# Kernel tuning notes

Measured on AMD Instinct MI355X. Metric: run time of the kernel, lower is better.

The kernel has to match this reference:

```python
import jax, jax.numpy as jnp
import numpy as np

TAU = 1.0  # confidence threshold (stands in for StatsTestConfidence)

BATCH = 8192
IN_FEATURES = 4096
OUT_FEATURES = 4096
EARLY_K = 1024


def setup_inputs() -> dict:
    key = jax.random.key(0)
    kx, kw = jax.random.split(key)
    x = jax.random.normal(kx, (BATCH, IN_FEATURES), dtype=jnp.float32)
    # nn.Linear weight: (out_features, in_features)
    W = jax.random.normal(kw, (OUT_FEATURES, IN_FEATURES), dtype=jnp.float32) * (IN_FEATURES ** -0.5)
    return {"x": x, "W": W, "early_terminate_it": EARLY_K}


def reference(x, W, early_terminate_it):
    k = early_terminate_it
    # partial matmul over first k input channels
    y1 = x[:, :k] @ W[:, :k].T                              # [B, out]
    # per-column squared rank-1 accumulation == (x^2) @ (W^2)^T over first k cols
    cum_squared = (x[:, :k] ** 2) @ (W[:, :k] ** 2).T        # [B, out]
    # confidence test: outputs whose partial sum is small relative to its
    # column-wise energy are 'passed' (early-terminated to 0)
    passed_mask = jnp.abs(y1) < TAU * jnp.sqrt(cum_squared)  # [B, out] bool
    # remaining matmul over the rest of the input channels
    y2 = x[:, k:] @ W[:, k:].T                               # [B, out]
    return jnp.where(passed_mask, jnp.zeros((), x.dtype), y1 + y2)
```

## Files before the change

### kernel.cpp

```cpp
#include <hip/hip_runtime.h>
#include <math.h>

#define BATCH 8192
#define OUTF  4096
#define INF   4096
#define K1    1024
#define KC    512
#define MARGIN 8.0e-4f

#define BK 32
#define NT (INF / BK)
#define NT1 (K1 / BK)
#define NP1 32
#define NSTEPS 80
#define GRIDX 32
#define GRIDY 64

typedef __attribute__((ext_vector_type(8))) short bf16x8;
typedef __attribute__((ext_vector_type(8))) unsigned short u16x8;
typedef __attribute__((ext_vector_type(4))) float f32x4;

__device__ inline unsigned short bf16_rn(float f) {
    unsigned u = __float_as_uint(f);
    unsigned r = 0x7FFFu + ((u >> 16) & 1u);
    return (unsigned short)((u + r) >> 16);
}
__device__ inline float bf16_f(unsigned short h) {
    return __uint_as_float(((unsigned)h) << 16);
}

__device__ inline int swz_idx(int r, int cc) {
    return r * 32 + ((cc ^ ((r >> 1) & 3)) << 3);
}

__device__ inline void gload_lds16(const void* g, void* l) {
    __builtin_amdgcn_global_load_lds(
        (const __attribute__((address_space(1))) unsigned*)g,
        (__attribute__((address_space(3))) unsigned*)l, 16, 0, 0);
}

__device__ float exact_serial(const float* __restrict__ x,
                              const float* __restrict__ w, int b, int o) {
    const float* xr = x + (size_t)b * INF;
    const float* wr = w + (size_t)o * INF;
    float py = 0.f, ty = 0.f, pc = 0.f, tcs = 0.f;
    double y1d = 0.0, y2d = 0.0;
    for (int j = 0; j < K1; ++j) {
        float xv = xr[j], wv = wr[j];
        py = fmaf(xv, wv, py);
        pc = fmaf(xv * xv, wv * wv, pc);
        y1d += (double)xv * (double)wv;
        if (((j + 1) & (KC - 1)) == 0) { ty += py; py = 0.f; tcs += pc; pc = 0.f; }
    }
    for (int j = K1; j < INF; ++j)
        y2d += (double)xr[j] * (double)wr[j];
    bool passed = fabsf(ty) < (float)sqrt((double)tcs);
    return passed ? 0.f : (float)(y1d + y2d);
}

__global__ void zero_ws(unsigned* ws) {
    if (threadIdx.x < 16) ws[threadIdx.x] = 0u;
}

__global__ __launch_bounds__(256) void
split_rows(const float* __restrict__ src, unsigned short* __restrict__ pair,
           unsigned short* __restrict__ sq, int nrows)
{
    int t = blockIdx.x * blockDim.x + threadIdx.x;
    if (t >= nrows * (INF / 8)) return;
    int gr  = t >> 9;
    int gk8 = t & 511;
    int kb = gk8 >> 2, cc = gk8 & 3;
    int rb = gr >> 7,  r  = gr & 127;
    int swz = swz_idx(r, cc);

    const float* s = src + (size_t)gr * INF + gk8 * 8;
    float4 f0 = *(const float4*)s;
    float4 f1 = *(const float4*)(s + 4);
    float fv[8] = {f0.x, f0.y, f0.z, f0.w, f1.x, f1.y, f1.z, f1.w};
    u16x8 h8, l8, s8;
    #pragma unroll
    for (int e = 0; e < 8; ++e) {
        float f = fv[e];
        unsigned short h = bf16_rn(f);
        h8[e] = h;
        l8[e] = bf16_rn(f - bf16_f(h));
        s8[e] = bf16_rn(f * f);
    }
    size_t pb = ((size_t)rb * (INF / 32) + kb) * 8192;
    *(u16x8*)&pair[pb + swz] = h8;
    if (kb < NT1) {
        *(u16x8*)&pair[pb + 4096 + swz] = l8;
        size_t qb = ((size_t)rb * NT1 + kb) * 4096;
        *(u16x8*)&sq[qb + swz] = s8;
    }
}

__global__ __launch_bounds__(256, 3) void
cs_kernel(const unsigned short* __restrict__ xsq,
          const unsigned short* __restrict__ wsq, float* __restrict__ out)
{
    __shared__ unsigned short lds2[16384];

    unsigned orig = blockIdx.y * GRIDX + blockIdx.x;
    unsigned swid = (orig & 7u) * (GRIDX * GRIDY / 8) + (orig >> 3);
    const int bx = (int)(swid & (GRIDX - 1));
    const int by = (int)(swid / GRIDX);
    const int brow = by * 128;
    const int bcol = bx * 128;

    const int tid  = threadIdx.x;
    const int lane = tid & 63;
    const int wvid = tid >> 6;
    const int wm   = wvid >> 1;
    const int wn   = wvid & 1;

    const int c0 = lane >> 4;
    int aidx[4], bidx[4];
    #pragma unroll
    for (int mi = 0; mi < 4; ++mi)
        aidx[mi] = swz_idx(wm * 64 + mi * 16 + (lane & 15), c0);
    #pragma unroll
    for (int nj = 0; nj < 4; ++nj)
        bidx[nj] = 4096 + swz_idx(wn * 64 + nj * 16 + (lane & 15), c0);

    f32x4 cs[4][4];
    #pragma unroll
    for (int mi = 0; mi < 4; ++mi)
        #pragma unroll
        for (int nj = 0; nj < 4; ++nj)
            cs[mi][nj] = (f32x4){0.f, 0.f, 0.f, 0.f};

    char* ldsb = (char*)lds2;
    const char* xq = (const char*)xsq + (size_t)by * NT1 * 8192;
    const char* wq = (const char*)wsq + (size_t)bx * NT1 * 8192;

    auto STAGE = [&](int dstB, int t) {
        #pragma unroll
        for (int i = 0; i < 4; ++i) {
            int j = wvid + i * 4;
            const char* g = (j < 8) ? xq + (size_t)t * 8192 + j * 1024
                                    : wq + (size_t)t * 8192 + (j - 8) * 1024;
            gload_lds16(g + lane * 16, ldsb + dstB + j * 1024);
        }
    };

    STAGE(0, 0);
    int bo = 0;
    for (int t = 0; t < NT1; ++t) {
        asm volatile("s_waitcnt vmcnt(0)" ::: "memory");
        __builtin_amdgcn_s_barrier();
        __builtin_amdgcn_sched_barrier(0);
        if (t + 1 < NT1) STAGE((bo ^ 8192) * 2, t + 1);

        bf16x8 b2[4];
        #pragma unroll
        for (int nj = 0; nj < 4; ++nj)
            b2[nj] = *(const bf16x8*)&lds2[bo + bidx[nj]];
        #pragma unroll
        for (int mi = 0; mi < 4; ++mi) {
            bf16x8 a2 = *(const bf16x8*)&lds2[bo + aidx[mi]];
            #pragma unroll
            for (int nj = 0; nj < 4; ++nj)
                cs[mi][nj] = __builtin_amdgcn_mfma_f32_16x16x32_bf16(a2, b2[nj], cs[mi][nj], 0, 0, 0);
        }
        bo ^= 8192;
    }

    const int rbase = brow + wm * 64 + (lane >> 4) * 4;
    const int cbase = bcol + wn * 64 + (lane & 15);
    #pragma unroll
    for (int mi = 0; mi < 4; ++mi)
        #pragma unroll
        for (int nj = 0; nj < 4; ++nj)
            #pragma unroll
            for (int q = 0; q < 4; ++q)
                out[(size_t)(rbase + mi * 16 + q) * OUTF + cbase + nj * 16] =
                    sqrtf(cs[mi][nj][q]);
}

__global__ __launch_bounds__(256, 2) void
mfma_pass_a9(const unsigned short* __restrict__ xpair,
             const unsigned short* __restrict__ wpair,
             const float* __restrict__ x, const float* __restrict__ w,
             float* __restrict__ out, unsigned* ws,
             unsigned* __restrict__ list, unsigned cap)
{
    __shared__ unsigned short lds_us[32768];

    unsigned orig = blockIdx.y * GRIDX + blockIdx.x;
    unsigned swid = (orig & 7u) * (GRIDX * GRIDY / 8) + (orig >> 3);
    const int bx = (int)(swid & (GRIDX - 1));
    const int by = (int)(swid / GRIDX);
    const int brow = by * 128;
    const int bcol = bx * 128;

    const int tid  = threadIdx.x;
    const int lane = tid & 63;
    const int wvid = tid >> 6;
    const int wm   = wvid >> 1;
    const int wn   = wvid & 1;

    const int c0 = lane >> 4;
    int aidx[4], bidx[4];
    #pragma unroll
    for (int mi = 0; mi < 4; ++mi)
        aidx[mi] = swz_idx(wm * 64 + mi * 16 + (lane & 15), c0);
    #pragma unroll
    for (int nj = 0; nj < 4; ++nj)
        bidx[nj] = swz_idx(wn * 64 + nj * 16 + (lane & 15), c0);

    const int rbase = brow + wm * 64 + (lane >> 4) * 4;
    const int cbase = bcol + wn * 64 + (lane & 15);

    f32x4 acc[4][4];
    #pragma unroll
    for (int mi = 0; mi < 4; ++mi)
        #pragma unroll
        for (int nj = 0; nj < 4; ++nj)
            acc[mi][nj] = (f32x4){0.f, 0.f, 0.f, 0.f};

    unsigned long long pmask = 0ull, nmask = 0ull;
    char* ldsb = (char*)lds_us;
    const char* xp = (const char*)xpair + (size_t)by * NT * 16384;
    const char* wp = (const char*)wpair + (size_t)bx * NT * 16384;

    auto STAGE = [&](int dstB, int s) {
        if (s < NP1) {
            #pragma unroll
            for (int i = 0; i < 8; ++i) {
                int j = wvid + i * 4;
                const char* g = (j < 16) ? xp + (size_t)s * 16384 + j * 1024
                                         : wp + (size_t)s * 16384 + (j - 16) * 1024;
                gload_lds16(g + lane * 16, ldsb + dstB + j * 1024);
            }
        } else {
            int kt = NT1 + 2 * (s - NP1);
            #pragma unroll
            for (int i = 0; i < 8; ++i) {
                int j = wvid + i * 4;
                const char* g =
                    (j < 8)  ? xp + (size_t)kt * 16384 + j * 1024 :
                    (j < 16) ? xp + (size_t)(kt + 1) * 16384 + (j - 8) * 1024 :
                    (j < 24) ? wp + (size_t)kt * 16384 + (j - 16) * 1024 :
                               wp + (size_t)(kt + 1) * 16384 + (j - 24) * 1024;
                gload_lds16(g + lane * 16, ldsb + dstB + j * 1024);
            }
        }
    };

    STAGE(0, 0);
    int bo = 0;
    for (int s = 0; s < NSTEPS; ++s) {
        asm volatile("s_waitcnt vmcnt(0)" ::: "memory");
        __builtin_amdgcn_s_barrier();
        __builtin_amdgcn_sched_barrier(0);

        if (s == NP1) {
            #pragma unroll
            for (int mi = 0; mi < 4; ++mi)
                #pragma unroll
                for (int nj = 0; nj < 4; ++nj)
                    #pragma unroll
                    for (int q = 0; q < 4; ++q) {
                        float sref = out[(size_t)(rbase + mi * 16 + q) * OUTF +
                                         cbase + nj * 16];
                        float d = fabsf(acc[mi][nj][q]) - sref;
                        int bit = ((mi * 4 + nj) * 4 + q);
                        if (d < 0.f)           pmask |= 1ull << bit;
                        if (fabsf(d) < MARGIN) nmask |= 1ull << bit;
                    }
        }

        if (s + 1 < NSTEPS) STAGE((bo ^ 16384) * 2, s + 1);

        if (s < NP1) {
            bf16x8 bh[4], bl[4];
            #pragma unroll
            for (int nj = 0; nj < 4; ++nj) {
                bh[nj] = *(const bf16x8*)&lds_us[bo + 8192  + bidx[nj]];
                bl[nj] = *(const bf16x8*)&lds_us[bo + 12288 + bidx[nj]];
            }
            #pragma unroll
            for (int mi = 0; mi < 4; ++mi) {
                bf16x8 ah = *(const bf16x8*)&lds_us[bo + aidx[mi]];
                bf16x8 al = *(const bf16x8*)&lds_us[bo + 4096 + aidx[mi]];
                #pragma unroll
                for (int nj = 0; nj < 4; ++nj) {
                    acc[mi][nj] = __builtin_amdgcn_mfma_f32_16x16x32_bf16(ah, bh[nj], acc[mi][nj], 0, 0, 0);
                    acc[mi][nj] = __builtin_amdgcn_mfma_f32_16x16x32_bf16(ah, bl[nj], acc[mi][nj], 0, 0, 0);
                    acc[mi][nj] = __builtin_amdgcn_mfma_f32_16x16x32_bf16(al, bh[nj], acc[mi][nj], 0, 0, 0);
                }
            }
        } else {
            #pragma unroll
            for (int sub = 0; sub < 2; ++sub) {
                const int ao = bo + sub * 4096;
                const int bb = bo + 8192 + sub * 4096;
                bf16x8 bh[4];
                #pragma unroll
                for (int nj = 0; nj < 4; ++nj)
                    bh[nj] = *(const bf16x8*)&lds_us[bb + bidx[nj]];
                #pragma unroll
                for (int mi = 0; mi < 4; ++mi) {
                    bf16x8 ah = *(const bf16x8*)&lds_us[ao + aidx[mi]];
                    #pragma unroll
                    for (int nj = 0; nj < 4; ++nj)
                        acc[mi][nj] = __builtin_amdgcn_mfma_f32_16x16x32_bf16(ah, bh[nj], acc[mi][nj], 0, 0, 0);
                }
            }
        }
        bo ^= 16384;
    }

    #pragma unroll
    for (int mi = 0; mi < 4; ++mi)
        #pragma unroll
        for (int nj = 0; nj < 4; ++nj) {
            int col = cbase + nj * 16;
            #pragma unroll
            for (int q = 0; q < 4; ++q) {
                int row = rbase + mi * 16 + q;
                int bit = ((mi * 4 + nj) * 4 + q);
                float raw = acc[mi][nj][q];
                float val = ((pmask >> bit) & 1ull) ? 0.f : raw;
                if ((nmask >> bit) & 1ull) {
                    unsigned idx = atomicAdd(&ws[0], 1u);
                    if (idx < cap) {
                        list[2 * idx]     = ((unsigned)row << 12) | (unsigned)col;
                        list[2 * idx + 1] = __float_as_uint(raw);
                    } else {
                        val = exact_serial(x, w, row, col);
                    }
                }
                out[(size_t)row * OUTF + col] = val;
            }
        }
}

__global__ __launch_bounds__(512) void
mfma_pass_a_fb(const float* __restrict__ x, const float* __restrict__ w,
               float* __restrict__ out, unsigned* ws,
               unsigned* __restrict__ list, unsigned cap)
{
    __shared__ unsigned short ldsA0[128 * 32];
    __shared__ unsigned short ldsA1[128 * 32];
    __shared__ unsigned short ldsA2[128 * 32];
    __shared__ unsigned short ldsB0[128 * 32];
    __shared__ unsigned short ldsB1[128 * 32];
    __shared__ unsigned short ldsB2[128 * 32];

    const int tid  = threadIdx.x;
    const int brow = blockIdx.y * 128;
    const int bcol = blockIdx.x * 128;
    const int lane = tid & 63;
    const int wid  = tid >> 6;
    const int wm   = wid >> 2;
    const int wn   = wid & 3;

    const int sr = tid >> 2;
    const int sc = tid & 3;
    const float* xg = x + (size_t)(brow + sr) * INF + sc * 8;
    const float* wg = w + (size_t)(bcol + sr) * INF + sc * 8;
    const int swz = sr * 32 + ((sc ^ (sr & 3)) << 3);

    const int c0 = lane >> 4;
    int aidx[4], bidx[2];
    #pragma unroll
    for (int mi = 0; mi < 4; ++mi) {
        int r = wm * 64 + mi * 16 + (lane & 15);
        aidx[mi] = r * 32 + ((c0 ^ (r & 3)) << 3);
    }
    #pragma unroll
    for (int nj = 0; nj < 2; ++nj) {
        int r = wn * 32 + nj * 16 + (lane & 15);
        bidx[nj] = r * 32 + ((c0 ^ (r & 3)) << 3);
    }

    f32x4 acc[4][2];
    f32x4 csa[4][2];
    #pragma unroll
    for (int mi = 0; mi < 4; ++mi)
        #pragma unroll
        for (int nj = 0; nj < 2; ++nj) {
            acc[mi][nj] = (f32x4){0.f, 0.f, 0.f, 0.f};
            csa[mi][nj] = (f32x4){0.f, 0.f, 0.f, 0.f};
        }

    for (int k0 = 0; k0 < K1; k0 += BK) {
        float xv[8], wv[8];
        *(float4*)&xv[0] = *(const float4*)(xg + k0);
        *(float4*)&xv[4] = *(const float4*)(xg + k0 + 4);
        *(float4*)&wv[0] = *(const float4*)(wg + k0);
        *(float4*)&wv[4] = *(const float4*)(wg + k0 + 4);
        __syncthreads();
        u16x8 h8, l8, s8;
        #pragma unroll
        for (int e = 0; e < 8; ++e) {
            float f = xv[e];
            unsigned short h = bf16_rn(f);
            h8[e] = h; l8[e] = bf16_rn(f - bf16_f(h)); s8[e] = bf16_rn(f * f);
        }
        *(u16x8*)&ldsA0[swz] = h8; *(u16x8*)&ldsA1[swz] = l8; *(u16x8*)&ldsA2[swz] = s8;
        #pragma unroll
        for (int e = 0; e < 8; ++e) {
            float f = wv[e];
            unsigned short h = bf16_rn(f);
            h8[e] = h; l8[e] = bf16_rn(f - bf16_f(h)); s8[e] = bf16_rn(f * f);
        }
        *(u16x8*)&ldsB0[swz] = h8; *(u16x8*)&ldsB1[swz] = l8; *(u16x8*)&ldsB2[swz] = s8;
        __syncthreads();

        bf16x8 bh[2], bl[2], b2[2];
        #pragma unroll
        for (int nj = 0; nj < 2; ++nj) {
            bh[nj] = *(const bf16x8*)&ldsB0[bidx[nj]];
            bl[nj] = *(const bf16x8*)&ldsB1[bidx[nj]];
            b2[nj] = *(const bf16x8*)&ldsB2[bidx[nj]];
        }
        #pragma unroll
        for (int mi = 0; mi < 4; ++mi) {
            bf16x8 ah = *(const bf16x8*)&ldsA0[aidx[mi]];
            bf16x8 al = *(const bf16x8*)&ldsA1[aidx[mi]];
            bf16x8 a2 = *(const bf16x8*)&ldsA2[aidx[mi]];
            #pragma unroll
            for (int nj = 0; nj < 2; ++nj) {
                acc[mi][nj] = __builtin_amdgcn_mfma_f32_16x16x32_bf16(ah, bh[nj], acc[mi][nj], 0, 0, 0);
                acc[mi][nj] = __builtin_amdgcn_mfma_f32_16x16x32_bf16(ah, bl[nj], acc[mi][nj], 0, 0, 0);
                acc[mi][nj] = __builtin_amdgcn_mfma_f32_16x16x32_bf16(al, bh[nj], acc[mi][nj], 0, 0, 0);
                csa[mi][nj] = __builtin_amdgcn_mfma_f32_16x16x32_bf16(a2, b2[nj], csa[mi][nj], 0, 0, 0);
            }
        }
    }

    unsigned pmask = 0u, nmask = 0u;
    #pragma unroll
    for (int mi = 0; mi < 4; ++mi)
        #pragma unroll
        for (int nj = 0; nj < 2; ++nj)
            #pragma unroll
            for (int q = 0; q < 4; ++q) {
                float d = fabsf(acc[mi][nj][q]) - sqrtf(csa[mi][nj][q]);
                unsigned bit = (unsigned)((((mi << 1) | nj) << 2) | q);
                if (d < 0.f)           pmask |= 1u << bit;
                if (fabsf(d) < MARGIN) nmask |= 1u << bit;
            }

    for (int k0 = K1; k0 < INF; k0 += BK) {
        float xv[8], wv[8];
        *(float4*)&xv[0] = *(const float4*)(xg + k0);
        *(float4*)&xv[4] = *(const float4*)(xg + k0 + 4);
        *(float4*)&wv[0] = *(const float4*)(wg + k0);
        *(float4*)&wv[4] = *(const float4*)(wg + k0 + 4);
        __syncthreads();
        u16x8 h8, l8;
        #pragma unroll
        for (int e = 0; e < 8; ++e) {
            float f = xv[e];
            unsigned short h = bf16_rn(f);
            h8[e] = h; l8[e] = bf16_rn(f - bf16_f(h));
        }
        *(u16x8*)&ldsA0[swz] = h8; *(u16x8*)&ldsA1[swz] = l8;
        #pragma unroll
        for (int e = 0; e < 8; ++e) {
            float f = wv[e];
            unsigned short h = bf16_rn(f);
            h8[e] = h; l8[e] = bf16_rn(f - bf16_f(h));
        }
        *(u16x8*)&ldsB0[swz] = h8; *(u16x8*)&ldsB1[swz] = l8;
        __syncthreads();

        bf16x8 bh[2], bl[2];
        #pragma unroll
        for (int nj = 0; nj < 2; ++nj) {
            bh[nj] = *(const bf16x8*)&ldsB0[bidx[nj]];
            bl[nj] = *(const bf16x8*)&ldsB1[bidx[nj]];
        }
        #pragma unroll
        for (int mi = 0; mi < 4; ++mi) {
            bf16x8 ah = *(const bf16x8*)&ldsA0[aidx[mi]];
            bf16x8 al = *(const bf16x8*)&ldsA1[aidx[mi]];
            #pragma unroll
            for (int nj = 0; nj < 2; ++nj) {
                acc[mi][nj] = __builtin_amdgcn_mfma_f32_16x16x32_bf16(ah, bh[nj], acc[mi][nj], 0, 0, 0);
                acc[mi][nj] = __builtin_amdgcn_mfma_f32_16x16x32_bf16(ah, bl[nj], acc[mi][nj], 0, 0, 0);
                acc[mi][nj] = __builtin_amdgcn_mfma_f32_16x16x32_bf16(al, bh[nj], acc[mi][nj], 0, 0, 0);
            }
        }
    }

    const int rbase = brow + wm * 64 + (lane >> 4) * 4;
    const int cbase = bcol + wn * 32 + (lane & 15);
    #pragma unroll
    for (int mi = 0; mi < 4; ++mi)
        #pragma unroll
        for (int nj = 0; nj < 2; ++nj) {
            int col = cbase + nj * 16;
            #pragma unroll
            for (int q = 0; q < 4; ++q) {
                int row = rbase + mi * 16 + q;
                unsigned bit = (unsigned)((((mi << 1) | nj) << 2) | q);
                float raw = acc[mi][nj][q];
                float val = ((pmask >> bit) & 1u) ? 0.f : raw;
                if ((nmask >> bit) & 1u) {
                    unsigned idx = ws ? atomicAdd(&ws[0], 1u) : 0xFFFFFFFFu;
                    if (idx < cap) {
                        list[2 * idx]     = ((unsigned)row << 12) | (unsigned)col;
                        list[2 * idx + 1] = __float_as_uint(raw);
                    } else {
                        val = exact_serial(x, w, row, col);
                    }
                }
                out[(size_t)row * OUTF + col] = val;
            }
        }
}

__global__ __launch_bounds__(256) void
exact_pass_b(const float* __restrict__ x, const float* __restrict__ w,
             float* __restrict__ out, const unsigned* __restrict__ ws,
             const unsigned* __restrict__ list, unsigned cap)
{
    unsigned n = ws[0]; if (n > cap) n = cap;
    unsigned stride = gridDim.x * blockDim.x;
    for (unsigned e = blockIdx.x * blockDim.x + threadIdx.x; e < n; e += stride) {
        unsigned p  = list[2 * e];
        float   val = __uint_as_float(list[2 * e + 1]);
        int b = (int)(p >> 12), o = (int)(p & 4095u);
        const float* xr = x + (size_t)b * INF;
        const float* wr = w + (size_t)o * INF;

        float py = 0.f, ty = 0.f, pc = 0.f, tcs = 0.f;
        for (int j = 0; j < K1; j += 4) {
            float4 xv = *(const float4*)(xr + j);
            float4 wv = *(const float4*)(wr + j);
            py = fmaf(xv.x, wv.x, py); pc = fmaf(xv.x * xv.x, wv.x * wv.x, pc);
            py = fmaf(xv.y, wv.y, py); pc = fmaf(xv.y * xv.y, wv.y * wv.y, pc);
            py = fmaf(xv.z, wv.z, py); pc = fmaf(xv.z * xv.z, wv.z * wv.z, pc);
            py = fmaf(xv.w, wv.w, py); pc = fmaf(xv.w * xv.w, wv.w * wv.w, pc);
            if (((j + 4) & (KC - 1)) == 0) {
                ty += py;  py = 0.f;
                tcs += pc; pc = 0.f;
            }
        }
        bool passed = fabsf(ty) < (float)sqrt((double)tcs);
        out[(size_t)b * OUTF + o] = passed ? 0.f : val;
    }
}

extern "C" void kernel_launch(void* const* d_in, const int* in_sizes, int n_in,
                              void* d_out, int out_size, void* d_ws, size_t ws_size,
                              hipStream_t stream)
{
    const float* x = (const float*)d_in[0];
    const float* w = (const float*)d_in[1];
    float* out = (float*)d_out;

    const size_t MB = 1ull << 20;
    if (ws_size >= 224 * MB) {
        unsigned* ws   = (unsigned*)d_ws;
        unsigned* list = ws + 16;
        unsigned  cap  = (unsigned)((8 * MB - 64) / 8);
        char* base = (char*)d_ws;
        unsigned short* xpair = (unsigned short*)(base + 8 * MB);
        unsigned short* wpair = (unsigned short*)(base + 136 * MB);
        unsigned short* xsq   = (unsigned short*)(base + 200 * MB);
        unsigned short* wsq   = (unsigned short*)(base + 216 * MB);

        zero_ws<<<1, 64, 0, stream>>>(ws);
        split_rows<<<(BATCH * (INF / 8)) / 256, 256, 0, stream>>>(x, xpair, xsq, BATCH);
        split_rows<<<(OUTF  * (INF / 8)) / 256, 256, 0, stream>>>(w, wpair, wsq, OUTF);
        cs_kernel<<<dim3(GRIDX, GRIDY), 256, 0, stream>>>(xsq, wsq, out);
        mfma_pass_a9<<<dim3(GRIDX, GRIDY), 256, 0, stream>>>(
            xpair, wpair, x, w, out, ws, list, cap);
        exact_pass_b<<<1024, 256, 0, stream>>>(x, w, out, ws, list, cap);
    } else if (ws_size >= (1u << 20)) {
        unsigned* ws   = (unsigned*)d_ws;
        unsigned* list = ws + 16;
        size_t c = (ws_size - 64) / 8;
        unsigned cap = (c > (size_t)(1u << 23)) ? (1u << 23) : (unsigned)c;
        zero_ws<<<1, 64, 0, stream>>>(ws);
        mfma_pass_a_fb<<<dim3(32, 64), 512, 0, stream>>>(x, w, out, ws, list, cap);
        exact_pass_b<<<1024, 256, 0, stream>>>(x, w, out, ws, list, cap);
    } else {
        mfma_pass_a_fb<<<dim3(32, 64), 512, 0, stream>>>(x, w, out, nullptr, nullptr, 0);
    }
}
```

Measured before the change: 1.090 ms.

## Split fused two-phase MFMA kernel into separate y1 and y2 kernels

Replaces the single 80-step kernel with two launches. The first handles the first K1 channels with the 3-term bf16 split, makes the pass/near decision and writes y1. The second is a lighter single-term kernel for the remaining channels; it uses half the LDS and allows 4 blocks per CU, then adds y2 to the stored y1 unless y1 is zero. Staging now uses precomputed pointers that are bumped each step, and the list stores only indices because exact_pass_b reads the value back from out. The cost is an extra full read and write of the output buffer between kernels. Also, when the near-list overflows, entries are no longer checked exactly, and a y1 that happens to be exactly zero is treated as passed.

```diff
diff --git a/kernel.cpp b/kernel.cpp
--- a/kernel.cpp
+++ b/kernel.cpp
@@ -11,8 +11,7 @@
 #define BK 32
 #define NT (INF / BK)
 #define NT1 (K1 / BK)
-#define NP1 32
-#define NSTEPS 80
+#define NT2 (NT - NT1)
 #define GRIDX 32
 #define GRIDY 64
 
@@ -37,25 +36,6 @@
     __builtin_amdgcn_global_load_lds(
         (const __attribute__((address_space(1))) unsigned*)g,
         (__attribute__((address_space(3))) unsigned*)l, 16, 0, 0);
-}
-
-__device__ float exact_serial(const float* __restrict__ x,
-                              const float* __restrict__ w, int b, int o) {
-    const float* xr = x + (size_t)b * INF;
-    const float* wr = w + (size_t)o * INF;
-    float py = 0.f, ty = 0.f, pc = 0.f, tcs = 0.f;
-    double y1d = 0.0, y2d = 0.0;
-    for (int j = 0; j < K1; ++j) {
-        float xv = xr[j], wv = wr[j];
-        py = fmaf(xv, wv, py);
-        pc = fmaf(xv * xv, wv * wv, pc);
-        y1d += (double)xv * (double)wv;
-        if (((j + 1) & (KC - 1)) == 0) { ty += py; py = 0.f; tcs += pc; pc = 0.f; }
-    }
-    for (int j = K1; j < INF; ++j)
-        y2d += (double)xr[j] * (double)wr[j];
-    bool passed = fabsf(ty) < (float)sqrt((double)tcs);
-    return passed ? 0.f : (float)(y1d + y2d);
 }
 
 __global__ void zero_ws(unsigned* ws) {
@@ -135,23 +115,30 @@
     const char* xq = (const char*)xsq + (size_t)by * NT1 * 8192;
     const char* wq = (const char*)wsq + (size_t)bx * NT1 * 8192;
 
-    auto STAGE = [&](int dstB, int t) {
-        #pragma unroll
-        for (int i = 0; i < 4; ++i) {
-            int j = wvid + i * 4;
-            const char* g = (j < 8) ? xq + (size_t)t * 8192 + j * 1024
-                                    : wq + (size_t)t * 8192 + (j - 8) * 1024;
-            gload_lds16(g + lane * 16, ldsb + dstB + j * 1024);
-        }
+    const char* gp[4];
+    #pragma unroll
+    for (int i = 0; i < 4; ++i) {
+        int j = wvid + i * 4;
+        gp[i] = ((j < 8) ? xq + j * 1024 : wq + (j - 8) * 1024) + lane * 16;
+    }
+
+    auto STAGE = [&](int dstB) {
+        #pragma unroll
+        for (int i = 0; i < 4; ++i)
+            gload_lds16(gp[i], ldsb + dstB + (wvid + i * 4) * 1024);
     };
-
-    STAGE(0, 0);
+    auto ADV = [&]() {
+        #pragma unroll
+        for (int i = 0; i < 4; ++i) gp[i] += 8192;
+    };
+
+    STAGE(0); ADV();
     int bo = 0;
     for (int t = 0; t < NT1; ++t) {
         asm volatile("s_waitcnt vmcnt(0)" ::: "memory");
         __builtin_amdgcn_s_barrier();
         __builtin_amdgcn_sched_barrier(0);
-        if (t + 1 < NT1) STAGE((bo ^ 8192) * 2, t + 1);
+        if (t + 1 < NT1) { STAGE((bo ^ 8192) * 2); ADV(); }
 
         bf16x8 b2[4];
         #pragma unroll
@@ -180,11 +167,10 @@
 }
 
 __global__ __launch_bounds__(256, 2) void
-mfma_pass_a9(const unsigned short* __restrict__ xpair,
-             const unsigned short* __restrict__ wpair,
-             const float* __restrict__ x, const float* __restrict__ w,
-             float* __restrict__ out, unsigned* ws,
-             unsigned* __restrict__ list, unsigned cap)
+mfma_p1(const unsigned short* __restrict__ xpair,
+        const unsigned short* __restrict__ wpair,
+        float* __restrict__ out, unsigned* ws,
+        unsigned* __restrict__ list, unsigned cap)
 {
     __shared__ unsigned short lds_us[32768];
 
@@ -220,94 +206,49 @@
         for (int nj = 0; nj < 4; ++nj)
             acc[mi][nj] = (f32x4){0.f, 0.f, 0.f, 0.f};
 
-    unsigned long long pmask = 0ull, nmask = 0ull;
     char* ldsb = (char*)lds_us;
     const char* xp = (const char*)xpair + (size_t)by * NT * 16384;
     const char* wp = (const char*)wpair + (size_t)bx * NT * 16384;
 
-    auto STAGE = [&](int dstB, int s) {
-        if (s < NP1) {
-            #pragma unroll
-            for (int i = 0; i < 8; ++i) {
-                int j = wvid + i * 4;
-                const char* g = (j < 16) ? xp + (size_t)s * 16384 + j * 1024
-                                         : wp + (size_t)s * 16384 + (j - 16) * 1024;
-                gload_lds16(g + lane * 16, ldsb + dstB + j * 1024);
-            }
-        } else {
-            int kt = NT1 + 2 * (s - NP1);
-            #pragma unroll
-            for (int i = 0; i < 8; ++i) {
-                int j = wvid + i * 4;
-                const char* g =
-                    (j < 8)  ? xp + (size_t)kt * 16384 + j * 1024 :
-                    (j < 16) ? xp + (size_t)(kt + 1) * 16384 + (j - 8) * 1024 :
-                    (j < 24) ? wp + (size_t)kt * 16384 + (j - 16) * 1024 :
-                               wp + (size_t)(kt + 1) * 16384 + (j - 24) * 1024;
-                gload_lds16(g + lane * 16, ldsb + dstB + j * 1024);
-            }
-        }
+    const char* gp[8];
+    #pragma unroll
+    for (int i = 0; i < 8; ++i) {
+        int j = wvid + i * 4;
+        gp[i] = ((j < 16) ? xp + j * 1024 : wp + (j - 16) * 1024) + lane * 16;
+    }
+    auto STAGE = [&](int dstB) {
+        #pragma unroll
+        for (int i = 0; i < 8; ++i)
+            gload_lds16(gp[i], ldsb + dstB + (wvid + i * 4) * 1024);
     };
-
-    STAGE(0, 0);
+    auto ADV = [&]() {
+        #pragma unroll
+        for (int i = 0; i < 8; ++i) gp[i] += 16384;
+    };
+
+    STAGE(0); ADV();
     int bo = 0;
-    for (int s = 0; s < NSTEPS; ++s) {
+    for (int s = 0; s < NT1; ++s) {
         asm volatile("s_waitcnt vmcnt(0)" ::: "memory");
         __builtin_amdgcn_s_barrier();
         __builtin_amdgcn_sched_barrier(0);
-
-        if (s == NP1) {
-            #pragma unroll
-            for (int mi = 0; mi < 4; ++mi)
-                #pragma unroll
-                for (int nj = 0; nj < 4; ++nj)
-                    #pragma unroll
-                    for (int q = 0; q < 4; ++q) {
-                        float sref = out[(size_t)(rbase + mi * 16 + q) * OUTF +
-                                         cbase + nj * 16];
-                        float d = fabsf(acc[mi][nj][q]) - sref;
-                        int bit = ((mi * 4 + nj) * 4 + q);
-                        if (d < 0.f)           pmask |= 1ull << bit;
-                        if (fabsf(d) < MARGIN) nmask |= 1ull << bit;
-                    }
-        }
-
-        if (s + 1 < NSTEPS) STAGE((bo ^ 16384) * 2, s + 1);
-
-        if (s < NP1) {
-            bf16x8 bh[4], bl[4];
+        if (s + 1 < NT1) { STAGE((bo ^ 16384) * 2); ADV(); }
+
+        bf16x8 bh[4], bl[4];
+        #pragma unroll
+        for (int nj = 0; nj < 4; ++nj) {
+            bh[nj] = *(const bf16x8*)&lds_us[bo + 8192  + bidx[nj]];
+            bl[nj] = *(const bf16x8*)&lds_us[bo + 12288 + bidx[nj]];
+        }
+        #pragma unroll
+        for (int mi = 0; mi < 4; ++mi) {
+            bf16x8 ah = *(const bf16x8*)&lds_us[bo + aidx[mi]];
+            bf16x8 al = *(const bf16x8*)&lds_us[bo + 4096 + aidx[mi]];
             #pragma unroll
             for (int nj = 0; nj < 4; ++nj) {
-                bh[nj] = *(const bf16x8*)&lds_us[bo + 8192  + bidx[nj]];
-                bl[nj] = *(const bf16x8*)&lds_us[bo + 12288 + bidx[nj]];
-            }
-            #pragma unroll
-            for (int mi = 0; mi < 4; ++mi) {
-                bf16x8 ah = *(const bf16x8*)&lds_us[bo + aidx[mi]];
-                bf16x8 al = *(const bf16x8*)&lds_us[bo + 4096 + aidx[mi]];
-                #pragma unroll
-                for (int nj = 0; nj < 4; ++nj) {
-                    acc[mi][nj] = __builtin_amdgcn_mfma_f32_16x16x32_bf16(ah, bh[nj], acc[mi][nj], 0, 0, 0);
-                    acc[mi][nj] = __builtin_amdgcn_mfma_f32_16x16x32_bf16(ah, bl[nj], acc[mi][nj], 0, 0, 0);
-                    acc[mi][nj] = __builtin_amdgcn_mfma_f32_16x16x32_bf16(al, bh[nj], acc[mi][nj], 0, 0, 0);
-                }
-            }
-        } else {
-            #pragma unroll
-            for (int sub = 0; sub < 2; ++sub) {
-                const int ao = bo + sub * 4096;
-                const int bb = bo + 8192 + sub * 4096;
-                bf16x8 bh[4];
-                #pragma unroll
-                for (int nj = 0; nj < 4; ++nj)
-                    bh[nj] = *(const bf16x8*)&lds_us[bb + bidx[nj]];
-                #pragma unroll
-                for (int mi = 0; mi < 4; ++mi) {
-                    bf16x8 ah = *(const bf16x8*)&lds_us[ao + aidx[mi]];
-                    #pragma unroll
-                    for (int nj = 0; nj < 4; ++nj)
-                        acc[mi][nj] = __builtin_amdgcn_mfma_f32_16x16x32_bf16(ah, bh[nj], acc[mi][nj], 0, 0, 0);
-                }
+                acc[mi][nj] = __builtin_amdgcn_mfma_f32_16x16x32_bf16(ah, bh[nj], acc[mi][nj], 0, 0, 0);
+                acc[mi][nj] = __builtin_amdgcn_mfma_f32_16x16x32_bf16(ah, bl[nj], acc[mi][nj], 0, 0, 0);
+                acc[mi][nj] = __builtin_amdgcn_mfma_f32_16x16x32_bf16(al, bh[nj], acc[mi][nj], 0, 0, 0);
             }
         }
         bo ^= 16384;
@@ -321,19 +262,114 @@
             #pragma unroll
             for (int q = 0; q < 4; ++q) {
                 int row = rbase + mi * 16 + q;
-                int bit = ((mi * 4 + nj) * 4 + q);
-                float raw = acc[mi][nj][q];
-                float val = ((pmask >> bit) & 1ull) ? 0.f : raw;
-                if ((nmask >> bit) & 1ull) {
-                    unsigned idx = atomicAdd(&ws[0], 1u);
-                    if (idx < cap) {
-                        list[2 * idx]     = ((unsigned)row << 12) | (unsigned)col;
-                        list[2 * idx + 1] = __float_as_uint(raw);
-                    } else {
-                        val = exact_serial(x, w, row, col);
-                    }
+                size_t idx = (size_t)row * OUTF + col;
+                float sref = out[idx];
+                float raw  = acc[mi][nj][q];
+                float d = fabsf(raw) - sref;
+                bool passed = d < 0.f;
+                bool near   = fabsf(d) < MARGIN;
+                if (near) {
+                    unsigned li = atomicAdd(&ws[0], 1u);
+                    if (li < cap)
+                        list[li] = ((unsigned)row << 12) | (unsigned)col;
                 }
-                out[(size_t)row * OUTF + col] = val;
+                out[idx] = (passed && !near) ? 0.f : raw;
+            }
+        }
+}
+
+__global__ __launch_bounds__(256, 4) void
+mfma_p2(const unsigned short* __restrict__ xpair,
+        const unsigned short* __restrict__ wpair,
+        float* __restrict__ out)
+{
+    __shared__ unsigned short lds_us[16384];
+
+    unsigned orig = blockIdx.y * GRIDX + blockIdx.x;
+    unsigned swid = (orig & 7u) * (GRIDX * GRIDY / 8) + (orig >> 3);
+    const int bx = (int)(swid & (GRIDX - 1));
+    const int by = (int)(swid / GRIDX);
+    const int brow = by * 128;
+    const int bcol = bx * 128;
+
+    const int tid  = threadIdx.x;
+    const int lane = tid & 63;
+    const int wvid = tid >> 6;
+    const int wm   = wvid >> 1;
+    const int wn   = wvid & 1;
+
+    const int c0 = lane >> 4;
+    int aidx[4], bidx[4];
+    #pragma unroll
+    for (int mi = 0; mi < 4; ++mi)
+        aidx[mi] = swz_idx(wm * 64 + mi * 16 + (lane & 15), c0);
+    #pragma unroll
+    for (int nj = 0; nj < 4; ++nj)
+        bidx[nj] = 4096 + swz_idx(wn * 64 + nj * 16 + (lane & 15), c0);
+
+    const int rbase = brow + wm * 64 + (lane >> 4) * 4;
+    const int cbase = bcol + wn * 64 + (lane & 15);
+
+    f32x4 acc[4][4];
+    #pragma unroll
+    for (int mi = 0; mi < 4; ++mi)
+        #pragma unroll
+        for (int nj = 0; nj < 4; ++nj)
+            acc[mi][nj] = (f32x4){0.f, 0.f, 0.f, 0.f};
+
+    char* ldsb = (char*)lds_us;
+    const char* xp = (const char*)xpair + ((size_t)by * NT + NT1) * 16384;
+    const char* wp = (const char*)wpair + ((size_t)bx * NT + NT1) * 16384;
+
+    const char* gp[4];
+    #pragma unroll
+    for (int i = 0; i < 4; ++i) {
+        int j = wvid + i * 4;
+        gp[i] = ((j < 8) ? xp + j * 1024 : wp + (j - 8) * 1024) + lane * 16;
+    }
+    auto STAGE = [&](int dstB) {
+        #pragma unroll
+        for (int i = 0; i < 4; ++i)
+            gload_lds16(gp[i], ldsb + dstB + (wvid + i * 4) * 1024);
+    };
+    auto ADV = [&]() {
+        #pragma unroll
+        for (int i = 0; i < 4; ++i) gp[i] += 16384;
+    };
+
+    STAGE(0); ADV();
+    int bo = 0;
+    for (int s = 0; s < NT2; ++s) {
+        asm volatile("s_waitcnt vmcnt(0)" ::: "memory");
+        __builtin_amdgcn_s_barrier();
+        __builtin_amdgcn_sched_barrier(0);
+        if (s + 1 < NT2) { STAGE((bo ^ 8192) * 2); ADV(); }
+
+        bf16x8 bh[4];
+        #pragma unroll
+        for (int nj = 0; nj < 4; ++nj)
+            bh[nj] = *(const bf16x8*)&lds_us[bo + bidx[nj]];
+        #pragma unroll
+        for (int mi = 0; mi < 4; ++mi) {
+            bf16x8 ah = *(const bf16x8*)&lds_us[bo + aidx[mi]];
+            #pragma unroll
+            for (int nj = 0; nj < 4; ++nj)
+                acc[mi][nj] = __builtin_amdgcn_mfma_f32_16x16x32_bf16(ah, bh[nj], acc[mi][nj], 0, 0, 0);
+        }
+        bo ^= 8192;
+    }
+
+    #pragma unroll
+    for (int mi = 0; mi < 4; ++mi)
+        #pragma unroll
+        for (int nj = 0; nj < 4; ++nj) {
+            int col = cbase + nj * 16;
+            #pragma unroll
+            for (int q = 0; q < 4; ++q) {
+                int row = rbase + mi * 16 + q;
+                size_t idx = (size_t)row * OUTF + col;
+                float y1v = out[idx];
+                out[idx] = (y1v == 0.f) ? 0.f : (y1v + acc[mi][nj][q]);
             }
         }
 }
@@ -501,17 +537,14 @@
                 int row = rbase + mi * 16 + q;
                 unsigned bit = (unsigned)((((mi << 1) | nj) << 2) | q);
                 float raw = acc[mi][nj][q];
-                float val = ((pmask >> bit) & 1u) ? 0.f : raw;
-                if ((nmask >> bit) & 1u) {
-                    unsigned idx = ws ? atomicAdd(&ws[0], 1u) : 0xFFFFFFFFu;
-                    if (idx < cap) {
-                        list[2 * idx]     = ((unsigned)row << 12) | (unsigned)col;
-                        list[2 * idx + 1] = __float_as_uint(raw);
-                    } else {
-                        val = exact_serial(x, w, row, col);
-                    }
+                bool passed = (pmask >> bit) & 1u;
+                bool near   = (nmask >> bit) & 1u;
+                if (near && ws) {
+                    unsigned li = atomicAdd(&ws[0], 1u);
+                    if (li < cap)
+                        list[li] = ((unsigned)row << 12) | (unsigned)col;
                 }
-                out[(size_t)row * OUTF + col] = val;
+                out[(size_t)row * OUTF + col] = (passed && !near) ? 0.f : raw;
             }
         }
 }
@@ -524,8 +557,7 @@
     unsigned n = ws[0]; if (n > cap) n = cap;
     unsigned stride = gridDim.x * blockDim.x;
     for (unsigned e = blockIdx.x * blockDim.x + threadIdx.x; e < n; e += stride) {
-        unsigned p  = list[2 * e];
-        float   val = __uint_as_float(list[2 * e + 1]);
+        unsigned p = list[e];
         int b = (int)(p >> 12), o = (int)(p & 4095u);
         const float* xr = x + (size_t)b * INF;
         const float* wr = w + (size_t)o * INF;
@@ -544,7 +576,8 @@
             }
         }
         bool passed = fabsf(ty) < (float)sqrt((double)tcs);
-        out[(size_t)b * OUTF + o] = passed ? 0.f : val;
+        size_t idx = (size_t)b * OUTF + o;
+        out[idx] = passed ? 0.f : out[idx];
     }
 }
 
@@ -560,7 +593,7 @@
     if (ws_size >= 224 * MB) {
         unsigned* ws   = (unsigned*)d_ws;
         unsigned* list = ws + 16;
-        unsigned  cap  = (unsigned)((8 * MB - 64) / 8);
+        unsigned  cap  = (unsigned)((8 * MB - 64) / 4);
         char* base = (char*)d_ws;
         unsigned short* xpair = (unsigned short*)(base + 8 * MB);
         unsigned short* wpair = (unsigned short*)(base + 136 * MB);
@@ -571,13 +604,13 @@
         split_rows<<<(BATCH * (INF / 8)) / 256, 256, 0, stream>>>(x, xpair, xsq, BATCH);
         split_rows<<<(OUTF  * (INF / 8)) / 256, 256, 0, stream>>>(w, wpair, wsq, OUTF);
         cs_kernel<<<dim3(GRIDX, GRIDY), 256, 0, stream>>>(xsq, wsq, out);
-        mfma_pass_a9<<<dim3(GRIDX, GRIDY), 256, 0, stream>>>(
-            xpair, wpair, x, w, out, ws, list, cap);
+        mfma_p1<<<dim3(GRIDX, GRIDY), 256, 0, stream>>>(xpair, wpair, out, ws, list, cap);
+        mfma_p2<<<dim3(GRIDX, GRIDY), 256, 0, stream>>>(xpair, wpair, out);
         exact_pass_b<<<1024, 256, 0, stream>>>(x, w, out, ws, list, cap);
     } else if (ws_size >= (1u << 20)) {
         unsigned* ws   = (unsigned*)d_ws;
         unsigned* list = ws + 16;
-        size_t c = (ws_size - 64) / 8;
+        size_t c = (ws_size - 64) / 4;
         unsigned cap = (c > (size_t)(1u << 23)) ? (1u << 23) : (unsigned)c;
         zero_ws<<<1, 64, 0, stream>>>(ws);
         mfma_pass_a_fb<<<dim3(32, 64), 512, 0, stream>>>(x, w, out, ws, list, cap);
```

Result: slower. 1.134 ms (+4.0%).

## Load low-bf16 residual fragments directly from global and shrink LDS footprint

Applied to the files above, without the earlier changes.

The main MFMA kernel no longer stages the low halves of the split-bf16 operands through LDS. split_rows now writes them in a per-lane fragment layout, so they can be read straight from global memory into registers. The tail loop goes back to one K-tile per step instead of two, LDS use is halved, and the occupancy hints are raised (3 blocks per CU for the main kernel, 4 for cs_kernel). The exact_serial fallback for list overflow is removed, so entries past capacity would keep the unrefined value, and the direct global loads add latency that is not double-buffered.

```diff
diff --git a/kernel.cpp b/kernel.cpp
--- a/kernel.cpp
+++ b/kernel.cpp
@@ -11,8 +11,6 @@
 #define BK 32
 #define NT (INF / BK)
 #define NT1 (K1 / BK)
-#define NP1 32
-#define NSTEPS 80
 #define GRIDX 32
 #define GRIDY 64
 
@@ -32,30 +30,14 @@
 __device__ inline int swz_idx(int r, int cc) {
     return r * 32 + ((cc ^ ((r >> 1) & 3)) << 3);
 }
+__device__ inline int frag_idx(int r, int cc) {
+    return ((r >> 4) * 64 + cc * 16 + (r & 15)) * 8;
+}
 
 __device__ inline void gload_lds16(const void* g, void* l) {
     __builtin_amdgcn_global_load_lds(
         (const __attribute__((address_space(1))) unsigned*)g,
         (__attribute__((address_space(3))) unsigned*)l, 16, 0, 0);
-}
-
-__device__ float exact_serial(const float* __restrict__ x,
-                              const float* __restrict__ w, int b, int o) {
-    const float* xr = x + (size_t)b * INF;
-    const float* wr = w + (size_t)o * INF;
-    float py = 0.f, ty = 0.f, pc = 0.f, tcs = 0.f;
-    double y1d = 0.0, y2d = 0.0;
-    for (int j = 0; j < K1; ++j) {
-        float xv = xr[j], wv = wr[j];
-        py = fmaf(xv, wv, py);
-        pc = fmaf(xv * xv, wv * wv, pc);
-        y1d += (double)xv * (double)wv;
-        if (((j + 1) & (KC - 1)) == 0) { ty += py; py = 0.f; tcs += pc; pc = 0.f; }
-    }
-    for (int j = K1; j < INF; ++j)
-        y2d += (double)xr[j] * (double)wr[j];
-    bool passed = fabsf(ty) < (float)sqrt((double)tcs);
-    return passed ? 0.f : (float)(y1d + y2d);
 }
 
 __global__ void zero_ws(unsigned* ws) {
@@ -72,7 +54,6 @@
     int gk8 = t & 511;
     int kb = gk8 >> 2, cc = gk8 & 3;
     int rb = gr >> 7,  r  = gr & 127;
-    int swz = swz_idx(r, cc);
 
     const float* s = src + (size_t)gr * INF + gk8 * 8;
     float4 f0 = *(const float4*)s;
@@ -88,15 +69,15 @@
         s8[e] = bf16_rn(f * f);
     }
     size_t pb = ((size_t)rb * (INF / 32) + kb) * 8192;
-    *(u16x8*)&pair[pb + swz] = h8;
+    *(u16x8*)&pair[pb + swz_idx(r, cc)] = h8;
     if (kb < NT1) {
-        *(u16x8*)&pair[pb + 4096 + swz] = l8;
+        *(u16x8*)&pair[pb + 4096 + frag_idx(r, cc)] = l8;
         size_t qb = ((size_t)rb * NT1 + kb) * 4096;
-        *(u16x8*)&sq[qb + swz] = s8;
-    }
-}
-
-__global__ __launch_bounds__(256, 3) void
+        *(u16x8*)&sq[qb + swz_idx(r, cc)] = s8;
+    }
+}
+
+__global__ __launch_bounds__(256, 4) void
 cs_kernel(const unsigned short* __restrict__ xsq,
           const unsigned short* __restrict__ wsq, float* __restrict__ out)
 {
@@ -179,14 +160,14 @@
                     sqrtf(cs[mi][nj][q]);
 }
 
-__global__ __launch_bounds__(256, 2) void
-mfma_pass_a9(const unsigned short* __restrict__ xpair,
-             const unsigned short* __restrict__ wpair,
-             const float* __restrict__ x, const float* __restrict__ w,
-             float* __restrict__ out, unsigned* ws,
-             unsigned* __restrict__ list, unsigned cap)
+__global__ __launch_bounds__(256, 3) void
+mfma_pa10(const unsigned short* __restrict__ xpair,
+          const unsigned short* __restrict__ wpair,
+          const float* __restrict__ x, const float* __restrict__ w,
+          float* __restrict__ out, unsigned* ws,
+          unsigned* __restrict__ list, unsigned cap)
 {
-    __shared__ unsigned short lds_us[32768];
+    __shared__ unsigned short lds_us[16384];
 
     unsigned orig = blockIdx.y * GRIDX + blockIdx.x;
     unsigned swid = (orig & 7u) * (GRIDX * GRIDY / 8) + (orig >> 3);
@@ -208,7 +189,7 @@
         aidx[mi] = swz_idx(wm * 64 + mi * 16 + (lane & 15), c0);
     #pragma unroll
     for (int nj = 0; nj < 4; ++nj)
-        bidx[nj] = swz_idx(wn * 64 + nj * 16 + (lane & 15), c0);
+        bidx[nj] = 4096 + swz_idx(wn * 64 + nj * 16 + (lane & 15), c0);
 
     const int rbase = brow + wm * 64 + (lane >> 4) * 4;
     const int cbase = bcol + wn * 64 + (lane & 15);
@@ -226,37 +207,23 @@
     const char* wp = (const char*)wpair + (size_t)bx * NT * 16384;
 
     auto STAGE = [&](int dstB, int s) {
-        if (s < NP1) {
-            #pragma unroll
-            for (int i = 0; i < 8; ++i) {
-                int j = wvid + i * 4;
-                const char* g = (j < 16) ? xp + (size_t)s * 16384 + j * 1024
-                                         : wp + (size_t)s * 16384 + (j - 16) * 1024;
-                gload_lds16(g + lane * 16, ldsb + dstB + j * 1024);
-            }
-        } else {
-            int kt = NT1 + 2 * (s - NP1);
-            #pragma unroll
-            for (int i = 0; i < 8; ++i) {
-                int j = wvid + i * 4;
-                const char* g =
-                    (j < 8)  ? xp + (size_t)kt * 16384 + j * 1024 :
-                    (j < 16) ? xp + (size_t)(kt + 1) * 16384 + (j - 8) * 1024 :
-                    (j < 24) ? wp + (size_t)kt * 16384 + (j - 16) * 1024 :
-                               wp + (size_t)(kt + 1) * 16384 + (j - 24) * 1024;
-                gload_lds16(g + lane * 16, ldsb + dstB + j * 1024);
-            }
+        #pragma unroll
+        for (int i = 0; i < 4; ++i) {
+            int j = wvid + i * 4;
+            const char* g = (j < 8) ? xp + (size_t)s * 16384 + j * 1024
+                                    : wp + (size_t)s * 16384 + (j - 8) * 1024;
+            gload_lds16(g + lane * 16, ldsb + dstB + j * 1024);
         }
     };
 
     STAGE(0, 0);
     int bo = 0;
-    for (int s = 0; s < NSTEPS; ++s) {
+    for (int s = 0; s < NT; ++s) {
         asm volatile("s_waitcnt vmcnt(0)" ::: "memory");
         __builtin_amdgcn_s_barrier();
         __builtin_amdgcn_sched_barrier(0);
 
-        if (s == NP1) {
+        if (s == NT1) {
             #pragma unroll
             for (int mi = 0; mi < 4; ++mi)
                 #pragma unroll
@@ -272,45 +239,47 @@
                     }
         }
 
-        if (s + 1 < NSTEPS) STAGE((bo ^ 16384) * 2, s + 1);
-
-        if (s < NP1) {
-            bf16x8 bh[4], bl[4];
-            #pragma unroll
-            for (int nj = 0; nj < 4; ++nj) {
-                bh[nj] = *(const bf16x8*)&lds_us[bo + 8192  + bidx[nj]];
-                bl[nj] = *(const bf16x8*)&lds_us[bo + 12288 + bidx[nj]];
-            }
+        if (s + 1 < NT) STAGE((bo ^ 8192) * 2, s + 1);
+
+        if (s < NT1) {
+            const char* xlo = xp + (size_t)s * 16384 + 8192 + lane * 16;
+            const char* wlo = wp + (size_t)s * 16384 + 8192 + lane * 16;
+            bf16x8 al[4], bl[4];
+            #pragma unroll
+            for (int mi = 0; mi < 4; ++mi)
+                al[mi] = *(const bf16x8*)(xlo + (wm * 4 + mi) * 1024);
+            #pragma unroll
+            for (int nj = 0; nj < 4; ++nj)
+                bl[nj] = *(const bf16x8*)(wlo + (wn * 4 + nj) * 1024);
+
+            bf16x8 bh[4];
+            #pragma unroll
+            for (int nj = 0; nj < 4; ++nj)
+                bh[nj] = *(const bf16x8*)&lds_us[bo + bidx[nj]];
             #pragma unroll
             for (int mi = 0; mi < 4; ++mi) {
                 bf16x8 ah = *(const bf16x8*)&lds_us[bo + aidx[mi]];
-                bf16x8 al = *(const bf16x8*)&lds_us[bo + 4096 + aidx[mi]];
                 #pragma unroll
                 for (int nj = 0; nj < 4; ++nj) {
                     acc[mi][nj] = __builtin_amdgcn_mfma_f32_16x16x32_bf16(ah, bh[nj], acc[mi][nj], 0, 0, 0);
                     acc[mi][nj] = __builtin_amdgcn_mfma_f32_16x16x32_bf16(ah, bl[nj], acc[mi][nj], 0, 0, 0);
-                    acc[mi][nj] = __builtin_amdgcn_mfma_f32_16x16x32_bf16(al, bh[nj], acc[mi][nj], 0, 0, 0);
+                    acc[mi][nj] = __builtin_amdgcn_mfma_f32_16x16x32_bf16(al[mi], bh[nj], acc[mi][nj], 0, 0, 0);
                 }
             }
         } else {
-            #pragma unroll
-            for (int sub = 0; sub < 2; ++sub) {
-                const int ao = bo + sub * 4096;
-                const int bb = bo + 8192 + sub * 4096;
-                bf16x8 bh[4];
+            bf16x8 bh[4];
+            #pragma unroll
+            for (int nj = 0; nj < 4; ++nj)
+                bh[nj] = *(const bf16x8*)&lds_us[bo + bidx[nj]];
+            #pragma unroll
+            for (int mi = 0; mi < 4; ++mi) {
+                bf16x8 ah = *(const bf16x8*)&lds_us[bo + aidx[mi]];
                 #pragma unroll
                 for (int nj = 0; nj < 4; ++nj)
-                    bh[nj] = *(const bf16x8*)&lds_us[bb + bidx[nj]];
-                #pragma unroll
-                for (int mi = 0; mi < 4; ++mi) {
-                    bf16x8 ah = *(const bf16x8*)&lds_us[ao + aidx[mi]];
-                    #pragma unroll
-                    for (int nj = 0; nj < 4; ++nj)
-                        acc[mi][nj] = __builtin_amdgcn_mfma_f32_16x16x32_bf16(ah, bh[nj], acc[mi][nj], 0, 0, 0);
-                }
-            }
-        }
-        bo ^= 16384;
+                    acc[mi][nj] = __builtin_amdgcn_mfma_f32_16x16x32_bf16(ah, bh[nj], acc[mi][nj], 0, 0, 0);
+            }
+        }
+        bo ^= 8192;
     }
 
     #pragma unroll
@@ -329,8 +298,6 @@
                     if (idx < cap) {
                         list[2 * idx]     = ((unsigned)row << 12) | (unsigned)col;
                         list[2 * idx + 1] = __float_as_uint(raw);
-                    } else {
-                        val = exact_serial(x, w, row, col);
                     }
                 }
                 out[(size_t)row * OUTF + col] = val;
@@ -507,8 +474,6 @@
                     if (idx < cap) {
                         list[2 * idx]     = ((unsigned)row << 12) | (unsigned)col;
                         list[2 * idx + 1] = __float_as_uint(raw);
-                    } else {
-                        val = exact_serial(x, w, row, col);
                     }
                 }
                 out[(size_t)row * OUTF + col] = val;
@@ -571,7 +536,7 @@
         split_rows<<<(BATCH * (INF / 8)) / 256, 256, 0, stream>>>(x, xpair, xsq, BATCH);
         split_rows<<<(OUTF  * (INF / 8)) / 256, 256, 0, stream>>>(w, wpair, wsq, OUTF);
         cs_kernel<<<dim3(GRIDX, GRIDY), 256, 0, stream>>>(xsq, wsq, out);
-        mfma_pass_a9<<<dim3(GRIDX, GRIDY), 256, 0, stream>>>(
+        mfma_pa10<<<dim3(GRIDX, GRIDY), 256, 0, stream>>>(
             xpair, wpair, x, w, out, ws, list, cap);
         exact_pass_b<<<1024, 256, 0, stream>>>(x, w, out, ws, list, cap);
     } else if (ws_size >= (1u << 20)) {
```

Result: slower. 1.330 ms (+22.1%).
